# Kernel tuning notes

Hardware: AMD Instinct MI355X
Metric: run time of the kernel (lower is better)

Reference implementation:

```python
import jax, jax.numpy as jnp
import numpy as np

N, E, F, R, S = 20000, 320000, 64, 8, 10
AVG_NEIGH = 16.0


def setup_inputs() -> dict:
    key = jax.random.key(0)
    ks = jax.random.split(key, 16)
    inp = {
        "vectors": jax.random.normal(ks[0], (E, 3), jnp.float32),
        "node_feats": jax.random.normal(ks[1], (N, F, 4), jnp.float32),  # [N, F, 1(0e)+3(1o)]
        "node_specie": jax.random.randint(ks[2], (N,), 0, S),
        "radial_embedding": jax.random.normal(ks[3], (E, R), jnp.float32),
        "senders": jax.random.randint(ks[4], (E,), 0, N),
        "receivers": jax.random.randint(ks[5], (E,), 0, N),
        # residual FullyConnectedTensorProduct(feats, one-hot species 0e) == species-dep. linear per l
        "W_res_s": jax.random.normal(ks[6], (S, F, F), jnp.float32),
        "W_res_v": jax.random.normal(ks[7], (S, F, F), jnp.float32),
        # interaction block: input linear per l
        "W_in_s": jax.random.normal(ks[8], (F, F), jnp.float32),
        "W_in_v": jax.random.normal(ks[9], (F, F), jnp.float32),
        # radial MLP -> 5 CG tensor-product path weights per channel
        "mlp_w1": jax.random.normal(ks[10], (R, 64), jnp.float32),
        "mlp_w2": jax.random.normal(ks[11], (64, 5 * F), jnp.float32) / 8.0,
        # interaction block: output linear per l
        "W_out_s": jax.random.normal(ks[12], (F, F), jnp.float32),
        "W_out_v": jax.random.normal(ks[13], (F, F), jnp.float32),
        # symmetric product basis (correlation 3), species-dependent term weights
        "W_prod_s": jax.random.normal(ks[14], (S, 5, F), jnp.float32) * 0.3,
        "W_prod_v": jax.random.normal(ks[15], (S, 4, F), jnp.float32) * 0.3,
    }
    k2 = jax.random.split(jax.random.key(1), 3)
    inp["W_lin_s"] = jax.random.normal(k2[0], (F, F), jnp.float32)
    inp["W_lin_v"] = jax.random.normal(k2[1], (F, F), jnp.float32)
    inp["W_read"] = jax.random.normal(k2[2], (F, 1), jnp.float32)
    return inp


def _forward(vectors, node_feats, node_specie, radial_embedding, senders, receivers,
             W_res_s, W_res_v, W_in_s, W_in_v, mlp_w1, mlp_w2, W_out_s, W_out_v,
             W_prod_s, W_prod_v, W_lin_s, W_lin_v, W_read):
    inv_sf = 1.0 / jnp.sqrt(jnp.float32(F))
    s = node_feats[..., 0]          # [N,F]   0e channels
    v = node_feats[..., 1:]         # [N,F,3] 1o channels

    # --- residual connection: FCTP(feats, one-hot species 0e attrs) -> species-gated linear per l
    res_s = jnp.einsum('nf,ngf->ng', s, W_res_s[node_specie]) * inv_sf
    res_v = jnp.einsum('nfc,ngf->ngc', v, W_res_v[node_specie]) * inv_sf

    # --- InteractionBlock ---
    h_s = (s @ W_in_s) * inv_sf
    h_v = jnp.einsum('nfc,fg->ngc', v, W_in_v) * inv_sf

    # spherical harmonics up to max_ell=1: Y0 = 1, Y1 = unit edge vector
    r = jnp.sqrt(jnp.sum(vectors * vectors, -1) + 1e-12)
    Y1 = vectors / r[:, None]                                # [E,3]

    # radial MLP produces per-edge weights for the 5 CG paths:
    # (0e x Y0 -> 0e), (1o . Y1 -> 0e), (0e x Y1 -> 1o), (1o x Y0 -> 1o), (1o x Y1 -> 1o, cross)
    w = (jax.nn.silu(radial_embedding @ mlp_w1) @ mlp_w2).reshape(-1, 5, F)  # [E,5,F]

    ss = h_s[senders]                                        # [E,F]
    sv = h_v[senders]                                        # [E,F,3]
    dot = jnp.einsum('efc,ec->ef', sv, Y1)                   # [E,F]
    m_s = w[:, 0] * ss + w[:, 1] * dot                       # [E,F]
    m_v = (w[:, 2] * ss)[:, :, None] * Y1[:, None, :] \
        + w[:, 3][:, :, None] * sv \
        + w[:, 4][:, :, None] * jnp.cross(sv, Y1[:, None, :])  # [E,F,3]

    agg_s = jnp.zeros_like(h_s).at[receivers].add(m_s) / AVG_NEIGH
    agg_v = jnp.zeros_like(h_v).at[receivers].add(m_v) / AVG_NEIGH
    a_s = (agg_s @ W_out_s) * inv_sf
    a_v = jnp.einsum('nfc,fg->ngc', agg_v, W_out_v) * inv_sf

    # --- EquivariantProductBasisBlock: correlation-3 symmetric contraction, species-dependent ---
    vv = jnp.sum(a_v * a_v, -1)                              # [N,F] invariant |v|^2
    Wp = W_prod_s[node_specie]                               # [N,5,F]
    p_s = (Wp[:, 0] * a_s + Wp[:, 1] * a_s ** 2 + Wp[:, 2] * a_s ** 3
           + Wp[:, 3] * vv + Wp[:, 4] * a_s * vv)
    Wv = W_prod_v[node_specie]                               # [N,4,F]
    p_v = (Wv[:, 0] + Wv[:, 1] * a_s + Wv[:, 2] * a_s ** 2 + Wv[:, 3] * vv)[:, :, None] * a_v

    f_s = (p_s @ W_lin_s) * inv_sf + res_s
    f_v = jnp.einsum('nfc,fg->ngc', p_v, W_lin_v) * inv_sf + res_v

    # --- LinearReadoutBlock (output_irreps = 0e), 1 head ---
    node_out = ((f_s @ W_read) * inv_sf)[:, None, :]         # [N, heads=1, 1]
    new_feats = jnp.concatenate([f_s[..., None], f_v], axis=-1)  # [N,F,4]
    return node_out, new_feats


def reference(vectors, node_feats, node_specie, radial_embedding, senders, receivers,
              W_res_s, W_res_v, W_in_s, W_in_v, mlp_w1, mlp_w2, W_out_s, W_out_v,
              W_prod_s, W_prod_v, W_lin_s, W_lin_v, W_read):
    return _forward(vectors, node_feats, node_specie, radial_embedding, senders, receivers,
                    W_res_s, W_res_v, W_in_s, W_in_v, mlp_w1, mlp_w2, W_out_s, W_out_v,
                    W_prod_s, W_prod_v, W_lin_s, W_lin_v, W_read)
```

## Files before the change

kernel.cpp:

```cpp
#include <hip/hip_runtime.h>
#include <math.h>

#define NN 20000
#define NE 320000
#define NF (NN*64)
#define TB 16

__device__ __forceinline__ float silu_f(float x){ return x / (1.0f + expf(-x)); }

__global__ __launch_bounds__(256) void k_transpose_res(
    const float* __restrict__ Ws, const float* __restrict__ Wv,
    float* __restrict__ Wst, float* __restrict__ Wvt)
{
  int i = blockIdx.x*256 + threadIdx.x;
  int spec = i >> 12;
  int g = (i >> 6) & 63;
  int f = i & 63;
  Wst[spec*4096 + f*64 + g] = Ws[i];
  Wvt[spec*4096 + f*64 + g] = Wv[i];
}

__global__ __launch_bounds__(256) void k_node_pre(
    const float* __restrict__ node_feats, const float* __restrict__ W_in_s,
    const float* __restrict__ W_in_v, float* __restrict__ h_s, float* __restrict__ h_v)
{
  __shared__ float sh[4][4][64];
  int wave = threadIdx.x >> 6, lane = threadIdx.x & 63;
  int n = blockIdx.x*4 + wave;
  int o = n*64 + lane;
  float4 nf = *(const float4*)(node_feats + (size_t)o*4);
  sh[wave][0][lane]=nf.x; sh[wave][1][lane]=nf.y; sh[wave][2][lane]=nf.z; sh[wave][3][lane]=nf.w;
  __syncthreads();
  float as=0.f, av0=0.f, av1=0.f, av2=0.f;
  #pragma unroll 8
  for(int f=0; f<64; ++f){
    float ws = W_in_s[f*64+lane], wv = W_in_v[f*64+lane];
    as  += sh[wave][0][f]*ws;
    av0 += sh[wave][1][f]*wv;
    av1 += sh[wave][2][f]*wv;
    av2 += sh[wave][3][f]*wv;
  }
  h_s[o]      = as *0.125f;
  h_v[o]      = av0*0.125f;
  h_v[NF+o]   = av1*0.125f;
  h_v[2*NF+o] = av2*0.125f;
}

__global__ __launch_bounds__(256) void k_edge(
    const float* __restrict__ vectors, const float* __restrict__ radial,
    const int* __restrict__ senders, const int* __restrict__ receivers,
    const float* __restrict__ mlp_w1, const float* __restrict__ mlp_w2,
    const float* __restrict__ h_s, const float* __restrict__ h_v,
    float* __restrict__ agg_s, float* __restrict__ agg_v)
{
  __shared__ float rad[4][128];
  __shared__ float hid[4][TB][64];
  int wave = threadIdx.x >> 6, lane = threadIdx.x & 63;
  int wgid = blockIdx.x*4 + wave;
  int e0 = wgid*TB;
  rad[wave][lane]    = radial[e0*8 + lane];
  rad[wave][64+lane] = radial[e0*8 + 64 + lane];
  __syncthreads();
  #pragma unroll
  for(int t=0;t<TB;++t){
    float acc=0.f;
    #pragma unroll
    for(int r=0;r<8;++r) acc += rad[wave][t*8+r]*mlp_w1[r*64+lane];
    hid[wave][t][lane] = silu_f(acc);
  }
  __syncthreads();
  float w[5][TB];
  #pragma unroll
  for(int j=0;j<5;++j)
    #pragma unroll
    for(int t=0;t<TB;++t) w[j][t]=0.f;
  for(int h=0; h<64; h+=2){
    float b0[5], b1[5];
    #pragma unroll
    for(int j=0;j<5;++j){
      b0[j]=mlp_w2[h*320     + j*64 + lane];
      b1[j]=mlp_w2[(h+1)*320 + j*64 + lane];
    }
    #pragma unroll
    for(int t=0;t<TB;++t){
      float2 hb = *(const float2*)&hid[wave][t][h];
      #pragma unroll
      for(int j=0;j<5;++j) w[j][t] = fmaf(hb.x, b0[j], fmaf(hb.y, b1[j], w[j][t]));
    }
  }
  #pragma unroll
  for(int t=0;t<TB;++t){
    int e = e0 + t;
    int snd = senders[e], rcv = receivers[e];
    float vx=vectors[e*3], vy=vectors[e*3+1], vz=vectors[e*3+2];
    float rinv = 1.0f/sqrtf(vx*vx+vy*vy+vz*vz+1e-12f);
    float y0=vx*rinv, y1=vy*rinv, y2=vz*rinv;
    int so = snd*64+lane, ro = rcv*64+lane;
    float ss  = h_s[so];
    float sv0 = h_v[so], sv1 = h_v[NF+so], sv2 = h_v[2*NF+so];
    float dot = sv0*y0 + sv1*y1 + sv2*y2;
    float ms  = w[0][t]*ss + w[1][t]*dot;
    float w2s = w[2][t]*ss, w3t = w[3][t], w4t = w[4][t];
    float mv0 = w2s*y0 + w3t*sv0 + w4t*(sv1*y2 - sv2*y1);
    float mv1 = w2s*y1 + w3t*sv1 + w4t*(sv2*y0 - sv0*y2);
    float mv2 = w2s*y2 + w3t*sv2 + w4t*(sv0*y1 - sv1*y0);
    atomicAdd(&agg_s[ro],      ms);
    atomicAdd(&agg_v[ro],      mv0);
    atomicAdd(&agg_v[NF+ro],   mv1);
    atomicAdd(&agg_v[2*NF+ro], mv2);
  }
}

__global__ __launch_bounds__(256) void k_node_post(
  const float* __restrict__ node_feats, const int* __restrict__ specie,
  const float* __restrict__ agg_s, const float* __restrict__ agg_v,
  const float* __restrict__ Wrst, const float* __restrict__ Wrvt,
  const float* __restrict__ W_out_s, const float* __restrict__ W_out_v,
  const float* __restrict__ W_prod_s, const float* __restrict__ W_prod_v,
  const float* __restrict__ W_lin_s, const float* __restrict__ W_lin_v,
  const float* __restrict__ W_read, float* __restrict__ out_node, float* __restrict__ out_feats)
{
  __shared__ float shA[4][4][64];
  __shared__ float shS[4][4][64];
  __shared__ float shP[4][4][64];
  int wave = threadIdx.x >> 6, lane = threadIdx.x & 63;
  int n = blockIdx.x*4 + wave;
  int o = n*64 + lane;
  shA[wave][0][lane] = agg_s[o]      * (1.f/16.f);
  shA[wave][1][lane] = agg_v[o]      * (1.f/16.f);
  shA[wave][2][lane] = agg_v[NF+o]   * (1.f/16.f);
  shA[wave][3][lane] = agg_v[2*NF+o] * (1.f/16.f);
  float4 nf = *(const float4*)(node_feats + (size_t)o*4);
  shS[wave][0][lane]=nf.x; shS[wave][1][lane]=nf.y; shS[wave][2][lane]=nf.z; shS[wave][3][lane]=nf.w;
  __syncthreads();
  int spec = specie[n];
  const float* Ws_ = Wrst + spec*4096;
  const float* Wv_ = Wrvt + spec*4096;
  float a_s=0.f,a0=0.f,a1=0.f,a2=0.f, r_s=0.f,r0=0.f,r1=0.f,r2=0.f;
  #pragma unroll 4
  for(int f=0; f<64; ++f){
    float wos=W_out_s[f*64+lane], wov=W_out_v[f*64+lane];
    a_s += shA[wave][0][f]*wos;
    a0  += shA[wave][1][f]*wov;
    a1  += shA[wave][2][f]*wov;
    a2  += shA[wave][3][f]*wov;
    float wrs=Ws_[f*64+lane], wrv=Wv_[f*64+lane];
    r_s += shS[wave][0][f]*wrs;
    r0  += shS[wave][1][f]*wrv;
    r1  += shS[wave][2][f]*wrv;
    r2  += shS[wave][3][f]*wrv;
  }
  a_s*=0.125f; a0*=0.125f; a1*=0.125f; a2*=0.125f;
  r_s*=0.125f; r0*=0.125f; r1*=0.125f; r2*=0.125f;
  float vv = a0*a0 + a1*a1 + a2*a2;
  float as2 = a_s*a_s;
  const float* Wp = W_prod_s + spec*320;
  float p_s = Wp[lane]*a_s + Wp[64+lane]*as2 + Wp[128+lane]*as2*a_s
            + Wp[192+lane]*vv + Wp[256+lane]*a_s*vv;
  const float* Wq = W_prod_v + spec*256;
  float coef = Wq[lane] + Wq[64+lane]*a_s + Wq[128+lane]*as2 + Wq[192+lane]*vv;
  shP[wave][0][lane] = p_s;
  shP[wave][1][lane] = coef*a0;
  shP[wave][2][lane] = coef*a1;
  shP[wave][3][lane] = coef*a2;
  __syncthreads();
  float fs=0.f,f0=0.f,f1=0.f,f2=0.f;
  #pragma unroll 4
  for(int f=0; f<64; ++f){
    float wls=W_lin_s[f*64+lane], wlv=W_lin_v[f*64+lane];
    fs += shP[wave][0][f]*wls;
    f0 += shP[wave][1][f]*wlv;
    f1 += shP[wave][2][f]*wlv;
    f2 += shP[wave][3][f]*wlv;
  }
  fs = fs*0.125f + r_s;
  f0 = f0*0.125f + r0;
  f1 = f1*0.125f + r1;
  f2 = f2*0.125f + r2;
  float x = fs * W_read[lane];
  #pragma unroll
  for(int off=32; off; off>>=1) x += __shfl_down(x, off);
  if(lane==0) out_node[n] = x*0.125f;
  float4 o4; o4.x=fs; o4.y=f0; o4.z=f1; o4.w=f2;
  *(float4*)(out_feats + (size_t)o*4) = o4;
}

extern "C" void kernel_launch(void* const* d_in, const int* in_sizes, int n_in,
                              void* d_out, int out_size, void* d_ws, size_t ws_size,
                              hipStream_t stream) {
  const float* vectors    = (const float*)d_in[0];
  const float* node_feats = (const float*)d_in[1];
  const int*   node_specie= (const int*)  d_in[2];
  const float* radial     = (const float*)d_in[3];
  const int*   senders    = (const int*)  d_in[4];
  const int*   receivers  = (const int*)  d_in[5];
  const float* W_res_s    = (const float*)d_in[6];
  const float* W_res_v    = (const float*)d_in[7];
  const float* W_in_s     = (const float*)d_in[8];
  const float* W_in_v     = (const float*)d_in[9];
  const float* mlp_w1     = (const float*)d_in[10];
  const float* mlp_w2     = (const float*)d_in[11];
  const float* W_out_s    = (const float*)d_in[12];
  const float* W_out_v    = (const float*)d_in[13];
  const float* W_prod_s   = (const float*)d_in[14];
  const float* W_prod_v   = (const float*)d_in[15];
  const float* W_lin_s    = (const float*)d_in[16];
  const float* W_lin_v    = (const float*)d_in[17];
  const float* W_read     = (const float*)d_in[18];

  float* ws   = (float*)d_ws;
  float* h_s  = ws;
  float* h_v  = ws + NF;
  float* agg_s= ws + 4*(size_t)NF;
  float* agg_v= ws + 5*(size_t)NF;
  float* Wrst = ws + 8*(size_t)NF;
  float* Wrvt = ws + 8*(size_t)NF + 40960;

  hipMemsetAsync(agg_s, 0, (size_t)4*NF*sizeof(float), stream);
  k_transpose_res<<<160, 256, 0, stream>>>(W_res_s, W_res_v, Wrst, Wrvt);
  k_node_pre<<<NN/4, 256, 0, stream>>>(node_feats, W_in_s, W_in_v, h_s, h_v);
  k_edge<<<NE/(4*TB), 256, 0, stream>>>(vectors, radial, senders, receivers,
                                        mlp_w1, mlp_w2, h_s, h_v, agg_s, agg_v);
  k_node_post<<<NN/4, 256, 0, stream>>>(node_feats, node_specie, agg_s, agg_v,
                                        Wrst, Wrvt, W_out_s, W_out_v,
                                        W_prod_s, W_prod_v, W_lin_s, W_lin_v,
                                        W_read, (float*)d_out, (float*)d_out + NN);
}
```

Baseline: 497.9 us.

## Use bf16x2 MFMA for edge radial MLP and batch nodes per wave

The edge kernel's second radial MLP layer now runs on MFMA 16x16x32 bf16 instructions. Hidden activations are split into hi and lo bf16 parts to recover near-fp32 accuracy, and mlp_w2 is pre-swizzled into bf16 fragment layout by a new prep kernel. Edge metadata and unit vectors are staged in shared memory, and the per-lane layout of the atomic scatter changes to match the MFMA output. The node pre and post kernels now process 8 nodes per wave so each weight load is reused across nodes. The trade-off is some precision loss because the weights are rounded to bf16, plus higher register pressure.

```diff
diff --git a/kernel.cpp b/kernel.cpp
--- a/kernel.cpp
+++ b/kernel.cpp
@@ -4,9 +4,35 @@
 #define NN 20000
 #define NE 320000
 #define NF (NN*64)
-#define TB 16
+
+typedef short sh8_t  __attribute__((ext_vector_type(8)));
+typedef float fl4_t  __attribute__((ext_vector_type(4)));
 
 __device__ __forceinline__ float silu_f(float x){ return x / (1.0f + expf(-x)); }
+
+__device__ __forceinline__ short f2bf(float f){
+  unsigned u = __builtin_bit_cast(unsigned, f);
+  unsigned r = (u + 0x7fffu + ((u >> 16) & 1u)) >> 16;
+  return (short)r;
+}
+__device__ __forceinline__ float bf2f(short s){
+  unsigned u = ((unsigned)(unsigned short)s) << 16;
+  return __builtin_bit_cast(float, u);
+}
+
+__global__ __launch_bounds__(256) void k_prep_w2(
+    const float* __restrict__ w2, short* __restrict__ w2f)
+{
+  int i = blockIdx.x*256 + threadIdx.x;
+  int jp   = i & 7;
+  int lane = (i >> 3) & 63;
+  int frag = i >> 9;
+  int k2 = frag / 20, p = frag % 20;
+  int j = p >> 2, T = p & 3;
+  int k = k2*32 + (lane >> 4)*8 + jp;
+  int n = j*64 + T*16 + (lane & 15);
+  w2f[i] = f2bf(w2[k*320 + n]);
+}
 
 __global__ __launch_bounds__(256) void k_transpose_res(
     const float* __restrict__ Ws, const float* __restrict__ Wv,
@@ -24,90 +50,120 @@
     const float* __restrict__ node_feats, const float* __restrict__ W_in_s,
     const float* __restrict__ W_in_v, float* __restrict__ h_s, float* __restrict__ h_v)
 {
-  __shared__ float sh[4][4][64];
+  __shared__ float4 sh[4][8][64];
   int wave = threadIdx.x >> 6, lane = threadIdx.x & 63;
-  int n = blockIdx.x*4 + wave;
-  int o = n*64 + lane;
-  float4 nf = *(const float4*)(node_feats + (size_t)o*4);
-  sh[wave][0][lane]=nf.x; sh[wave][1][lane]=nf.y; sh[wave][2][lane]=nf.z; sh[wave][3][lane]=nf.w;
-  __syncthreads();
-  float as=0.f, av0=0.f, av1=0.f, av2=0.f;
-  #pragma unroll 8
+  int n0 = blockIdx.x*32 + wave*8;
+  #pragma unroll
+  for(int nd=0; nd<8; ++nd)
+    sh[wave][nd][lane] = *(const float4*)(node_feats + ((size_t)(n0+nd)*64 + lane)*4);
+  float as[8], av0[8], av1[8], av2[8];
+  #pragma unroll
+  for(int nd=0; nd<8; ++nd){ as[nd]=0.f; av0[nd]=0.f; av1[nd]=0.f; av2[nd]=0.f; }
   for(int f=0; f<64; ++f){
     float ws = W_in_s[f*64+lane], wv = W_in_v[f*64+lane];
-    as  += sh[wave][0][f]*ws;
-    av0 += sh[wave][1][f]*wv;
-    av1 += sh[wave][2][f]*wv;
-    av2 += sh[wave][3][f]*wv;
-  }
-  h_s[o]      = as *0.125f;
-  h_v[o]      = av0*0.125f;
-  h_v[NF+o]   = av1*0.125f;
-  h_v[2*NF+o] = av2*0.125f;
+    #pragma unroll
+    for(int nd=0; nd<8; ++nd){
+      float4 t = sh[wave][nd][f];
+      as[nd]  += t.x*ws;
+      av0[nd] += t.y*wv;
+      av1[nd] += t.z*wv;
+      av2[nd] += t.w*wv;
+    }
+  }
+  #pragma unroll
+  for(int nd=0; nd<8; ++nd){
+    int o = (n0+nd)*64 + lane;
+    h_s[o]      = as[nd] *0.125f;
+    h_v[o]      = av0[nd]*0.125f;
+    h_v[NF+o]   = av1[nd]*0.125f;
+    h_v[2*NF+o] = av2[nd]*0.125f;
+  }
 }
 
 __global__ __launch_bounds__(256) void k_edge(
     const float* __restrict__ vectors, const float* __restrict__ radial,
     const int* __restrict__ senders, const int* __restrict__ receivers,
-    const float* __restrict__ mlp_w1, const float* __restrict__ mlp_w2,
+    const float* __restrict__ mlp_w1, const short* __restrict__ w2f,
     const float* __restrict__ h_s, const float* __restrict__ h_v,
     float* __restrict__ agg_s, float* __restrict__ agg_v)
 {
+  __shared__ float hid[4][16][68];
+  __shared__ float ey[4][16][3];
+  __shared__ int   esr[4][16][2];
   __shared__ float rad[4][128];
-  __shared__ float hid[4][TB][64];
   int wave = threadIdx.x >> 6, lane = threadIdx.x & 63;
-  int wgid = blockIdx.x*4 + wave;
-  int e0 = wgid*TB;
+  int e0 = blockIdx.x*64 + wave*16;
+
   rad[wave][lane]    = radial[e0*8 + lane];
   rad[wave][64+lane] = radial[e0*8 + 64 + lane];
-  __syncthreads();
-  #pragma unroll
-  for(int t=0;t<TB;++t){
-    float acc=0.f;
-    #pragma unroll
-    for(int r=0;r<8;++r) acc += rad[wave][t*8+r]*mlp_w1[r*64+lane];
+  if(lane < 16){
+    int e = e0 + lane;
+    float vx = vectors[3*e], vy = vectors[3*e+1], vz = vectors[3*e+2];
+    float rinv = 1.0f/sqrtf(vx*vx + vy*vy + vz*vz + 1e-12f);
+    ey[wave][lane][0]=vx*rinv; ey[wave][lane][1]=vy*rinv; ey[wave][lane][2]=vz*rinv;
+    esr[wave][lane][0]=senders[e]; esr[wave][lane][1]=receivers[e];
+  }
+  float w1r[8];
+  #pragma unroll
+  for(int r=0; r<8; ++r) w1r[r] = mlp_w1[r*64+lane];
+  #pragma unroll
+  for(int t=0; t<16; ++t){
+    float acc = 0.f;
+    #pragma unroll
+    for(int r=0; r<8; ++r) acc += rad[wave][t*8+r]*w1r[r];
     hid[wave][t][lane] = silu_f(acc);
   }
-  __syncthreads();
-  float w[5][TB];
-  #pragma unroll
-  for(int j=0;j<5;++j)
-    #pragma unroll
-    for(int t=0;t<TB;++t) w[j][t]=0.f;
-  for(int h=0; h<64; h+=2){
-    float b0[5], b1[5];
-    #pragma unroll
-    for(int j=0;j<5;++j){
-      b0[j]=mlp_w2[h*320     + j*64 + lane];
-      b1[j]=mlp_w2[(h+1)*320 + j*64 + lane];
-    }
-    #pragma unroll
-    for(int t=0;t<TB;++t){
-      float2 hb = *(const float2*)&hid[wave][t][h];
-      #pragma unroll
-      for(int j=0;j<5;++j) w[j][t] = fmaf(hb.x, b0[j], fmaf(hb.y, b1[j], w[j][t]));
-    }
-  }
-  #pragma unroll
-  for(int t=0;t<TB;++t){
-    int e = e0 + t;
-    int snd = senders[e], rcv = receivers[e];
-    float vx=vectors[e*3], vy=vectors[e*3+1], vz=vectors[e*3+2];
-    float rinv = 1.0f/sqrtf(vx*vx+vy*vy+vz*vz+1e-12f);
-    float y0=vx*rinv, y1=vy*rinv, y2=vz*rinv;
-    int so = snd*64+lane, ro = rcv*64+lane;
-    float ss  = h_s[so];
-    float sv0 = h_v[so], sv1 = h_v[NF+so], sv2 = h_v[2*NF+so];
-    float dot = sv0*y0 + sv1*y1 + sv2*y2;
-    float ms  = w[0][t]*ss + w[1][t]*dot;
-    float w2s = w[2][t]*ss, w3t = w[3][t], w4t = w[4][t];
-    float mv0 = w2s*y0 + w3t*sv0 + w4t*(sv1*y2 - sv2*y1);
-    float mv1 = w2s*y1 + w3t*sv1 + w4t*(sv2*y0 - sv0*y2);
-    float mv2 = w2s*y2 + w3t*sv2 + w4t*(sv0*y1 - sv1*y0);
-    atomicAdd(&agg_s[ro],      ms);
-    atomicAdd(&agg_v[ro],      mv0);
-    atomicAdd(&agg_v[NF+ro],   mv1);
-    atomicAdd(&agg_v[2*NF+ro], mv2);
+
+  fl4_t C[20];
+  #pragma unroll
+  for(int p=0; p<20; ++p) C[p] = (fl4_t){0.f,0.f,0.f,0.f};
+  int l15 = lane & 15, q = lane >> 4;
+  #pragma unroll
+  for(int k2=0; k2<2; ++k2){
+    const float* hp = &hid[wave][l15][k2*32 + q*8];
+    float a[8];
+    #pragma unroll
+    for(int i=0; i<8; ++i) a[i] = hp[i];
+    sh8_t ahi, alo;
+    #pragma unroll
+    for(int i=0; i<8; ++i){
+      short h = f2bf(a[i]);
+      ahi[i] = h;
+      alo[i] = f2bf(a[i] - bf2f(h));
+    }
+    const short* bbase = w2f + (size_t)(k2*20)*512 + lane*8;
+    #pragma unroll
+    for(int p=0; p<20; ++p){
+      sh8_t b = *(const sh8_t*)(bbase + p*512);
+      C[p] = __builtin_amdgcn_mfma_f32_16x16x32_bf16(ahi, b, C[p], 0, 0, 0);
+      C[p] = __builtin_amdgcn_mfma_f32_16x16x32_bf16(alo, b, C[p], 0, 0, 0);
+    }
+  }
+
+  #pragma unroll
+  for(int reg=0; reg<4; ++reg){
+    int r = q*4 + reg;
+    float y0 = ey[wave][r][0], y1 = ey[wave][r][1], y2 = ey[wave][r][2];
+    int snd = esr[wave][r][0], rcv = esr[wave][r][1];
+    #pragma unroll
+    for(int T=0; T<4; ++T){
+      int c = T*16 + l15;
+      int so = snd*64 + c, ro = rcv*64 + c;
+      float ss  = h_s[so];
+      float sv0 = h_v[so], sv1 = h_v[NF+so], sv2 = h_v[2*NF+so];
+      float dot = sv0*y0 + sv1*y1 + sv2*y2;
+      float w0 = C[T][reg], w1v = C[4+T][reg], w2v = C[8+T][reg];
+      float w3v = C[12+T][reg], w4v = C[16+T][reg];
+      float ms  = w0*ss + w1v*dot;
+      float w2s = w2v*ss;
+      float mv0 = w2s*y0 + w3v*sv0 + w4v*(sv1*y2 - sv2*y1);
+      float mv1 = w2s*y1 + w3v*sv1 + w4v*(sv2*y0 - sv0*y2);
+      float mv2 = w2s*y2 + w3v*sv2 + w4v*(sv0*y1 - sv1*y0);
+      atomicAdd(&agg_s[ro],      ms);
+      atomicAdd(&agg_v[ro],      mv0);
+      atomicAdd(&agg_v[NF+ro],   mv1);
+      atomicAdd(&agg_v[2*NF+ro], mv2);
+    }
   }
 }
 
@@ -120,69 +176,88 @@
   const float* __restrict__ W_lin_s, const float* __restrict__ W_lin_v,
   const float* __restrict__ W_read, float* __restrict__ out_node, float* __restrict__ out_feats)
 {
-  __shared__ float shA[4][4][64];
-  __shared__ float shS[4][4][64];
-  __shared__ float shP[4][4][64];
+  __shared__ float4 buf[4][8][64];
   int wave = threadIdx.x >> 6, lane = threadIdx.x & 63;
-  int n = blockIdx.x*4 + wave;
-  int o = n*64 + lane;
-  shA[wave][0][lane] = agg_s[o]      * (1.f/16.f);
-  shA[wave][1][lane] = agg_v[o]      * (1.f/16.f);
-  shA[wave][2][lane] = agg_v[NF+o]   * (1.f/16.f);
-  shA[wave][3][lane] = agg_v[2*NF+o] * (1.f/16.f);
-  float4 nf = *(const float4*)(node_feats + (size_t)o*4);
-  shS[wave][0][lane]=nf.x; shS[wave][1][lane]=nf.y; shS[wave][2][lane]=nf.z; shS[wave][3][lane]=nf.w;
-  __syncthreads();
-  int spec = specie[n];
-  const float* Ws_ = Wrst + spec*4096;
-  const float* Wv_ = Wrvt + spec*4096;
-  float a_s=0.f,a0=0.f,a1=0.f,a2=0.f, r_s=0.f,r0=0.f,r1=0.f,r2=0.f;
-  #pragma unroll 4
+  int n0 = blockIdx.x*32 + wave*8;
+  int sp[8];
+  #pragma unroll
+  for(int nd=0; nd<8; ++nd) sp[nd] = specie[n0+nd];
+
+  #pragma unroll
+  for(int nd=0; nd<8; ++nd){
+    int o = (n0+nd)*64 + lane;
+    buf[wave][nd][lane] = make_float4(agg_s[o]*(1.f/16.f), agg_v[o]*(1.f/16.f),
+                                      agg_v[NF+o]*(1.f/16.f), agg_v[2*NF+o]*(1.f/16.f));
+  }
+  float a_s[8], a0[8], a1[8], a2[8];
+  #pragma unroll
+  for(int nd=0; nd<8; ++nd){ a_s[nd]=0.f; a0[nd]=0.f; a1[nd]=0.f; a2[nd]=0.f; }
   for(int f=0; f<64; ++f){
-    float wos=W_out_s[f*64+lane], wov=W_out_v[f*64+lane];
-    a_s += shA[wave][0][f]*wos;
-    a0  += shA[wave][1][f]*wov;
-    a1  += shA[wave][2][f]*wov;
-    a2  += shA[wave][3][f]*wov;
-    float wrs=Ws_[f*64+lane], wrv=Wv_[f*64+lane];
-    r_s += shS[wave][0][f]*wrs;
-    r0  += shS[wave][1][f]*wrv;
-    r1  += shS[wave][2][f]*wrv;
-    r2  += shS[wave][3][f]*wrv;
-  }
-  a_s*=0.125f; a0*=0.125f; a1*=0.125f; a2*=0.125f;
-  r_s*=0.125f; r0*=0.125f; r1*=0.125f; r2*=0.125f;
-  float vv = a0*a0 + a1*a1 + a2*a2;
-  float as2 = a_s*a_s;
-  const float* Wp = W_prod_s + spec*320;
-  float p_s = Wp[lane]*a_s + Wp[64+lane]*as2 + Wp[128+lane]*as2*a_s
-            + Wp[192+lane]*vv + Wp[256+lane]*a_s*vv;
-  const float* Wq = W_prod_v + spec*256;
-  float coef = Wq[lane] + Wq[64+lane]*a_s + Wq[128+lane]*as2 + Wq[192+lane]*vv;
-  shP[wave][0][lane] = p_s;
-  shP[wave][1][lane] = coef*a0;
-  shP[wave][2][lane] = coef*a1;
-  shP[wave][3][lane] = coef*a2;
-  __syncthreads();
-  float fs=0.f,f0=0.f,f1=0.f,f2=0.f;
-  #pragma unroll 4
+    float wos = W_out_s[f*64+lane], wov = W_out_v[f*64+lane];
+    #pragma unroll
+    for(int nd=0; nd<8; ++nd){
+      float4 t = buf[wave][nd][f];
+      a_s[nd] += t.x*wos; a0[nd] += t.y*wov; a1[nd] += t.z*wov; a2[nd] += t.w*wov;
+    }
+  }
+  #pragma unroll
+  for(int nd=0; nd<8; ++nd){ a_s[nd]*=0.125f; a0[nd]*=0.125f; a1[nd]*=0.125f; a2[nd]*=0.125f; }
+
+  #pragma unroll
+  for(int nd=0; nd<8; ++nd)
+    buf[wave][nd][lane] = *(const float4*)(node_feats + ((size_t)(n0+nd)*64 + lane)*4);
+  float r_s[8], r0[8], r1[8], r2[8];
+  #pragma unroll
+  for(int nd=0; nd<8; ++nd){ r_s[nd]=0.f; r0[nd]=0.f; r1[nd]=0.f; r2[nd]=0.f; }
   for(int f=0; f<64; ++f){
-    float wls=W_lin_s[f*64+lane], wlv=W_lin_v[f*64+lane];
-    fs += shP[wave][0][f]*wls;
-    f0 += shP[wave][1][f]*wlv;
-    f1 += shP[wave][2][f]*wlv;
-    f2 += shP[wave][3][f]*wlv;
-  }
-  fs = fs*0.125f + r_s;
-  f0 = f0*0.125f + r0;
-  f1 = f1*0.125f + r1;
-  f2 = f2*0.125f + r2;
-  float x = fs * W_read[lane];
-  #pragma unroll
-  for(int off=32; off; off>>=1) x += __shfl_down(x, off);
-  if(lane==0) out_node[n] = x*0.125f;
-  float4 o4; o4.x=fs; o4.y=f0; o4.z=f1; o4.w=f2;
-  *(float4*)(out_feats + (size_t)o*4) = o4;
+    #pragma unroll
+    for(int nd=0; nd<8; ++nd){
+      float wrs = Wrst[sp[nd]*4096 + f*64 + lane];
+      float wrv = Wrvt[sp[nd]*4096 + f*64 + lane];
+      float4 t = buf[wave][nd][f];
+      r_s[nd] += t.x*wrs; r0[nd] += t.y*wrv; r1[nd] += t.z*wrv; r2[nd] += t.w*wrv;
+    }
+  }
+  #pragma unroll
+  for(int nd=0; nd<8; ++nd){ r_s[nd]*=0.125f; r0[nd]*=0.125f; r1[nd]*=0.125f; r2[nd]*=0.125f; }
+
+  #pragma unroll
+  for(int nd=0; nd<8; ++nd){
+    float vv = a0[nd]*a0[nd] + a1[nd]*a1[nd] + a2[nd]*a2[nd];
+    float as2 = a_s[nd]*a_s[nd];
+    const float* Wp = W_prod_s + sp[nd]*320;
+    float p_s = Wp[lane]*a_s[nd] + Wp[64+lane]*as2 + Wp[128+lane]*as2*a_s[nd]
+              + Wp[192+lane]*vv + Wp[256+lane]*a_s[nd]*vv;
+    const float* Wq = W_prod_v + sp[nd]*256;
+    float coef = Wq[lane] + Wq[64+lane]*a_s[nd] + Wq[128+lane]*as2 + Wq[192+lane]*vv;
+    buf[wave][nd][lane] = make_float4(p_s, coef*a0[nd], coef*a1[nd], coef*a2[nd]);
+  }
+  float fs[8], f0[8], f1[8], f2[8];
+  #pragma unroll
+  for(int nd=0; nd<8; ++nd){ fs[nd]=0.f; f0[nd]=0.f; f1[nd]=0.f; f2[nd]=0.f; }
+  for(int f=0; f<64; ++f){
+    float wls = W_lin_s[f*64+lane], wlv = W_lin_v[f*64+lane];
+    #pragma unroll
+    for(int nd=0; nd<8; ++nd){
+      float4 t = buf[wave][nd][f];
+      fs[nd] += t.x*wls; f0[nd] += t.y*wlv; f1[nd] += t.z*wlv; f2[nd] += t.w*wlv;
+    }
+  }
+  float wr = W_read[lane];
+  #pragma unroll
+  for(int nd=0; nd<8; ++nd){
+    float vs = fs[nd]*0.125f + r_s[nd];
+    float v0 = f0[nd]*0.125f + r0[nd];
+    float v1 = f1[nd]*0.125f + r1[nd];
+    float v2 = f2[nd]*0.125f + r2[nd];
+    int o = (n0+nd)*64 + lane;
+    float4 o4; o4.x=vs; o4.y=v0; o4.z=v1; o4.w=v2;
+    *(float4*)(out_feats + (size_t)o*4) = o4;
+    float x = vs * wr;
+    #pragma unroll
+    for(int off=32; off; off>>=1) x += __shfl_down(x, off);
+    if(lane==0) out_node[n0+nd] = x*0.125f;
+  }
 }
 
 extern "C" void kernel_launch(void* const* d_in, const int* in_sizes, int n_in,
@@ -215,14 +290,16 @@
   float* agg_v= ws + 5*(size_t)NF;
   float* Wrst = ws + 8*(size_t)NF;
   float* Wrvt = ws + 8*(size_t)NF + 40960;
+  short* w2f  = (short*)(ws + 8*(size_t)NF + 81920);
 
   hipMemsetAsync(agg_s, 0, (size_t)4*NF*sizeof(float), stream);
+  k_prep_w2<<<80, 256, 0, stream>>>(mlp_w2, w2f);
   k_transpose_res<<<160, 256, 0, stream>>>(W_res_s, W_res_v, Wrst, Wrvt);
-  k_node_pre<<<NN/4, 256, 0, stream>>>(node_feats, W_in_s, W_in_v, h_s, h_v);
-  k_edge<<<NE/(4*TB), 256, 0, stream>>>(vectors, radial, senders, receivers,
-                                        mlp_w1, mlp_w2, h_s, h_v, agg_s, agg_v);
-  k_node_post<<<NN/4, 256, 0, stream>>>(node_feats, node_specie, agg_s, agg_v,
-                                        Wrst, Wrvt, W_out_s, W_out_v,
-                                        W_prod_s, W_prod_v, W_lin_s, W_lin_v,
-                                        W_read, (float*)d_out, (float*)d_out + NN);
-}
+  k_node_pre<<<625, 256, 0, stream>>>(node_feats, W_in_s, W_in_v, h_s, h_v);
+  k_edge<<<NE/64, 256, 0, stream>>>(vectors, radial, senders, receivers,
+                                    mlp_w1, w2f, h_s, h_v, agg_s, agg_v);
+  k_node_post<<<625, 256, 0, stream>>>(node_feats, node_specie, agg_s, agg_v,
+                                       Wrst, Wrvt, W_out_s, W_out_v,
+                                       W_prod_s, W_prod_v, W_lin_s, W_lin_v,
+                                       W_read, (float*)d_out, (float*)d_out + NN);
+}
```

After: 541.7 us. 8.8% more time.
